# Performance work log

Measured on AMD Instinct MI355X. Metric: run time of the kernel, lower is better.

Reference implementation:

```python
import jax, jax.numpy as jnp
import numpy as np

EPS = 1e-12  # F.normalize default eps


def setup_inputs() -> dict:
    key = jax.random.key(0)
    k1, k2, k3, k4 = jax.random.split(key, 4)
    B, C, H, W = 8, 256, 128, 128
    N, T = 100, 6
    return {
        "visual_features": jax.random.normal(k1, (B, C, H, W), dtype=jnp.float32),
        "text_embeddings": jax.random.normal(k2, (T, C), dtype=jnp.float32),
        "masks": jax.random.uniform(k3, (B, N, H, W), dtype=jnp.float32),
        "class_labels": jax.random.randint(k4, (B, N), 0, 7),
        "temperature": jnp.asarray(0.07, dtype=jnp.float32),
    }


def reference(visual_features, text_embeddings, masks, class_labels, temperature):
    # visual_features: (B,C,H,W); text_embeddings: (T,C); masks: (B,N,H,W); class_labels: (B,N)
    T = text_embeddings.shape[0]
    # masks already at (H,W): bilinear resize to same size is identity -> just threshold
    mask_bin = (masks > 0.5).astype(visual_features.dtype)          # (B,N,H,W), detached
    mask_bin = jax.lax.stop_gradient(mask_bin)
    msum = mask_bin.sum(axis=(2, 3))                                 # (B,N)
    # masked sum-pool then mean (clamp denom at 1, as in torch)
    pooled = jnp.einsum('bchw,bnhw->bnc', visual_features, mask_bin)
    pooled = pooled / jnp.maximum(msum, 1.0)[..., None]              # (B,N,C)
    pooled = pooled / jnp.maximum(jnp.linalg.norm(pooled, axis=-1, keepdims=True), EPS)
    text_norm = text_embeddings / jnp.maximum(
        jnp.linalg.norm(text_embeddings, axis=-1, keepdims=True), EPS)
    sims = jnp.einsum('bnc,tc->bnt', pooled, text_norm) / jnp.abs(temperature)  # (B,N,T)
    logp = jax.nn.log_softmax(sims, axis=-1)
    tgt = jnp.clip(class_labels - 1, 0, T - 1)
    ce = -jnp.take_along_axis(logp, tgt[..., None], axis=-1)[..., 0]  # (B,N)
    valid = ((class_labels >= 1) & (class_labels <= T) & (msum >= 1.0)).astype(ce.dtype)
    cnt = valid.sum()
    loss = jnp.where(cnt > 0, (ce * valid).sum() / jnp.maximum(cnt, 1.0),
                     jnp.asarray(0.0, ce.dtype))
    return loss
```

## Files before the change

### kernel.cpp

```cpp
#include <hip/hip_runtime.h>
#include <hip/hip_bf16.h>
#include <stdint.h>

constexpr int cB  = 8;
constexpr int cC  = 256;
constexpr int cHW = 128 * 128;
constexpr int cN  = 100;
constexpr int cT  = 6;
constexpr int NPAD = 112;
constexpr int WPB = cHW / 32;
constexpr int KSLICES = 16;
constexpr int PXS = cHW / KSLICES;
constexpr int NWAVES = cB * 16 * KSLICES;

typedef __attribute__((ext_vector_type(8))) short short8;
typedef __attribute__((ext_vector_type(4))) float floatx4;

__device__ __forceinline__ unsigned pack2(float a, float b) {
    const __hip_bfloat16 ha = __float2bfloat16(a);
    const __hip_bfloat16 hb = __float2bfloat16(b);
    return (unsigned)__builtin_bit_cast(unsigned short, ha)
         | ((unsigned)__builtin_bit_cast(unsigned short, hb) << 16);
}

__global__ __launch_bounds__(256)
void mask_prep_kernel(const float* __restrict__ masks,
                      unsigned* __restrict__ bits, unsigned* __restrict__ msum)
{
    const int t = threadIdx.x, lane = t & 63, w = t >> 6;
    const int b = blockIdx.x / NPAD;
    const int n = blockIdx.x % NPAD;
    unsigned* dst = bits + ((size_t)b * NPAD + n) * WPB;

    if (n >= cN) {
        *(uint2*)(dst + t * 2) = make_uint2(0u, 0u);
        return;
    }
    const float* src = masks + ((size_t)b * cN + n) * cHW + w * 4096;
    unsigned* wdst = dst + w * 128;
    int pc = 0;
    for (int r = 0; r < 16; ++r) {
        const floatx4 v = *(const floatx4*)(src + r * 256 + lane * 4);
        const bool b0 = v.x > 0.5f, b1 = v.y > 0.5f, b2 = v.z > 0.5f, b3 = v.w > 0.5f;
        const unsigned long long B0 = __ballot(b0), B1 = __ballot(b1),
                                 B2 = __ballot(b2), B3 = __ballot(b3);
        pc += (int)b0 + (int)b1 + (int)b2 + (int)b3;
        if (lane < 8) {
            const int sh = lane * 8;
            const unsigned word =
                  (unsigned)((B0 >> sh) & 0xFFull)
                | ((unsigned)((B1 >> sh) & 0xFFull) << 8)
                | ((unsigned)((B2 >> sh) & 0xFFull) << 16)
                | ((unsigned)((B3 >> sh) & 0xFFull) << 24);
            wdst[r * 8 + lane] = word;
        }
    }
    #pragma unroll
    for (int off = 32; off > 0; off >>= 1) pc += __shfl_xor(pc, off, 64);
    __shared__ int ps[4];
    if (lane == 0) ps[w] = pc;
    __syncthreads();
    if (t == 0) msum[b * cN + n] = (unsigned)(ps[0] + ps[1] + ps[2] + ps[3]);
}

template<bool USE_PART>
__global__ __launch_bounds__(256)
void pool_kernel(const float* __restrict__ vf, const unsigned* __restrict__ bits,
                 float* __restrict__ part, float* __restrict__ pooled)
{
    const int tid  = threadIdx.x;
    const int lane = tid & 63;
    const int gw   = blockIdx.x * 4 + (tid >> 6);
    const int b    = gw >> 8;
    const int ct   = (gw >> 4) & 15;
    const int ks   = gw & 15;
    const int l15  = lane & 15;
    const int lk   = lane >> 4;
    const int lk2  = lk * 2;
    const int p0   = ks * PXS;

    const float* vrow = vf + ((size_t)(b * cC + ct * 16 + l15)) * cHW + p0 + lk * 8;
    const unsigned* brow = bits + ((size_t)b * NPAD + l15) * WPB + (p0 >> 5);

    floatx4 acc[7];
    #pragma unroll
    for (int mt = 0; mt < 7; ++mt) acc[mt] = (floatx4){0.f, 0.f, 0.f, 0.f};

    floatx4 vr[4][2];
    #pragma unroll
    for (int u = 0; u < 4; ++u) {
        vr[u][0] = *(const floatx4*)(vrow + u * 32);
        vr[u][1] = *(const floatx4*)(vrow + u * 32 + 4);
    }
    uint4 bwA[7], bwB[7];
    #pragma unroll
    for (int mt = 0; mt < 7; ++mt)
        bwA[mt] = *(const uint4*)(brow + (size_t)mt * 16 * WPB);

    auto GROUP = [&](int g, uint4 (&bw)[7], uint4 (&bwn)[7]) {
        if (g < 7) {
            #pragma unroll
            for (int mt = 0; mt < 7; ++mt)
                bwn[mt] = *(const uint4*)(brow + (size_t)mt * 16 * WPB + (g + 1) * 4);
        }
        #pragma unroll
        for (int u = 0; u < 4; ++u) {
            const int w = g * 4 + u;
            union { short8 s8; uint4 u4; } bq;
            bq.u4.x = pack2(vr[u][0].x, vr[u][0].y);
            bq.u4.y = pack2(vr[u][0].z, vr[u][0].w);
            bq.u4.z = pack2(vr[u][1].x, vr[u][1].y);
            bq.u4.w = pack2(vr[u][1].z, vr[u][1].w);
            if (g < 7) {
                vr[u][0] = *(const floatx4*)(vrow + (w + 4) * 32);
                vr[u][1] = *(const floatx4*)(vrow + (w + 4) * 32 + 4);
            }
            #pragma unroll
            for (int mt = 0; mt < 7; ++mt) {
                const unsigned word = (u == 0) ? bw[mt].x : (u == 1) ? bw[mt].y
                                    : (u == 2) ? bw[mt].z : bw[mt].w;
                const unsigned te = (word >> lk2) & 0x01010101u;
                const unsigned to = (word >> (lk2 + 1)) & 0x01010101u;
                union { short8 s8; uint4 u4; } aq;
                aq.u4.x = __umul24(__builtin_amdgcn_perm(0u, te, 0x04010400u), 0x3F80u);
                aq.u4.y = __umul24(__builtin_amdgcn_perm(0u, te, 0x04030402u), 0x3F80u);
                aq.u4.z = __umul24(__builtin_amdgcn_perm(0u, to, 0x04010400u), 0x3F80u);
                aq.u4.w = __umul24(__builtin_amdgcn_perm(0u, to, 0x04030402u), 0x3F80u);
                acc[mt] = __builtin_amdgcn_mfma_f32_16x16x32_bf16(aq.s8, bq.s8, acc[mt], 0, 0, 0);
            }
        }
    };

    for (int gp = 0; gp < 4; ++gp) {
        GROUP(2 * gp,     bwA, bwB);
        GROUP(2 * gp + 1, bwB, bwA);
    }

    if (USE_PART) {
        float* dst = part + (size_t)gw * (cN * 16);
        #pragma unroll
        for (int mt = 0; mt < 7; ++mt) {
            #pragma unroll
            for (int i = 0; i < 4; ++i) {
                const int n = mt * 16 + lk * 4 + i;
                if (n < cN) dst[n * 16 + l15] = acc[mt][i];
            }
        }
    } else {
        #pragma unroll
        for (int mt = 0; mt < 7; ++mt) {
            #pragma unroll
            for (int i = 0; i < 4; ++i) {
                const int n = mt * 16 + lk * 4 + i;
                if (n < cN)
                    atomicAdd(&pooled[((size_t)b * cN + n) * cC + ct * 16 + l15], acc[mt][i]);
            }
        }
    }
}

__device__ __forceinline__ float wred(float v) {
    #pragma unroll
    for (int off = 32; off > 0; off >>= 1) v += __shfl_xor(v, off, 64);
    return v;
}

template<bool USE_PART>
__global__ __launch_bounds__(256)
void finalize_kernel(const float* __restrict__ pp, const unsigned* __restrict__ msum,
                     const float* __restrict__ text, const int* __restrict__ labels,
                     const float* __restrict__ temp, float* __restrict__ bpart)
{
    const int lane = threadIdx.x & 63;
    const int wv   = threadIdx.x >> 6;
    const int row  = blockIdx.x * 4 + wv;
    const int b = row / cN, n = row % cN;

    floatx4 p = (floatx4){0.f, 0.f, 0.f, 0.f};
    if (USE_PART) {
        const int ct  = lane >> 2;
        const int col = (lane & 3) * 4;
        const float* src = pp + ((size_t)(b * 256 + ct * 16)) * (cN * 16) + n * 16 + col;
        #pragma unroll
        for (int kk = 0; kk < KSLICES; ++kk)
            p += *(const floatx4*)(src + (size_t)kk * (cN * 16));
    } else {
        p = *(const floatx4*)(pp + (size_t)row * cC + lane * 4);
    }

    const float m   = (float)msum[row];
    const float inv = 1.0f / fmaxf(m, 1.0f);
    p.x *= inv; p.y *= inv; p.z *= inv; p.w *= inv;

    const int c_global = USE_PART ? ((lane >> 2) * 16 + (lane & 3) * 4) : lane * 4;

    float psq = p.x * p.x + p.y * p.y + p.z * p.z + p.w * p.w;
    float dot[cT], tsq[cT];
    #pragma unroll
    for (int t = 0; t < cT; ++t) {
        const floatx4 x = *(const floatx4*)(text + (size_t)t * cC + c_global);
        dot[t] = p.x * x.x + p.y * x.y + p.z * x.z + p.w * x.w;
        tsq[t] = x.x * x.x + x.y * x.y + x.z * x.z + x.w * x.w;
    }
    psq = wred(psq);
    #pragma unroll
    for (int t = 0; t < cT; ++t) { dot[t] = wred(dot[t]); tsq[t] = wred(tsq[t]); }

    __shared__ float lce[4], lcnt[4];
    if (lane == 0) {
        const float tempv = fabsf(temp[0]);
        const float pn = fmaxf(sqrtf(psq), 1e-12f);
        float sims[cT], mx = -1e30f;
        #pragma unroll
        for (int t = 0; t < cT; ++t) {
            sims[t] = dot[t] / (pn * fmaxf(sqrtf(tsq[t]), 1e-12f)) / tempv;
            mx = fmaxf(mx, sims[t]);
        }
        float se = 0.f;
        #pragma unroll
        for (int t = 0; t < cT; ++t) se += expf(sims[t] - mx);
        const float lse = logf(se);

        const int lab = labels[row];
        const int tgt = min(max(lab - 1, 0), cT - 1);
        const float ce = -(sims[tgt] - mx - lse);
        const bool valid = (lab >= 1) && (lab <= cT) && (m >= 1.0f);
        lce[wv]  = valid ? ce : 0.f;
        lcnt[wv] = valid ? 1.f : 0.f;
    }
    __syncthreads();
    if (threadIdx.x == 0) {
        bpart[blockIdx.x * 2]     = lce[0] + lce[1] + lce[2] + lce[3];
        bpart[blockIdx.x * 2 + 1] = lcnt[0] + lcnt[1] + lcnt[2] + lcnt[3];
    }
}

__global__ __launch_bounds__(256)
void loss_kernel(const float* __restrict__ bp, float* __restrict__ out) {
    const int t = threadIdx.x, lane = t & 63, w = t >> 6;
    float ce = 0.f, cnt = 0.f;
    if (t < 200) { ce = bp[t * 2]; cnt = bp[t * 2 + 1]; }
    ce = wred(ce); cnt = wred(cnt);
    __shared__ float a[8];
    if (lane == 0) { a[w * 2] = ce; a[w * 2 + 1] = cnt; }
    __syncthreads();
    if (t == 0) {
        const float s = a[0] + a[2] + a[4] + a[6];
        const float c = a[1] + a[3] + a[5] + a[7];
        out[0] = (c > 0.f) ? s / fmaxf(c, 1.f) : 0.f;
    }
}

__global__ void zero_kernel(float* __restrict__ p, int n) {
    const int i = blockIdx.x * 256 + threadIdx.x;
    if (i < n) p[i] = 0.f;
}

extern "C" void kernel_launch(void* const* d_in, const int* in_sizes, int n_in,
                              void* d_out, int out_size, void* d_ws, size_t ws_size,
                              hipStream_t stream)
{
    const float* vf     = (const float*)d_in[0];
    const float* text   = (const float*)d_in[1];
    const float* masks  = (const float*)d_in[2];
    const int*   labels = (const int*)d_in[3];
    const float* temp   = (const float*)d_in[4];

    float*    wsf   = (float*)d_ws;
    float*    bpart = wsf;
    unsigned* msum  = (unsigned*)(wsf + 512);

    const size_t PART_FLOATS = (size_t)NWAVES * cN * 16;
    const size_t BITS_WORDS  = (size_t)cB * NPAD * WPB;

    const bool use_part =
        ws_size >= (4096 + PART_FLOATS + BITS_WORDS + 64) * sizeof(float);

    if (use_part) {
        float*    part = wsf + 4096;
        unsigned* bits = (unsigned*)(wsf + 4096 + PART_FLOATS);
        hipLaunchKernelGGL(mask_prep_kernel, dim3(cB * NPAD), dim3(256), 0, stream,
                           masks, bits, msum);
        hipLaunchKernelGGL((pool_kernel<true>), dim3(NWAVES / 4), dim3(256), 0, stream,
                           vf, bits, part, nullptr);
        hipLaunchKernelGGL((finalize_kernel<true>), dim3(cB * cN / 4), dim3(256), 0, stream,
                           part, msum, text, labels, temp, bpart);
    } else {
        float*    pooled = wsf + 4096;
        unsigned* bits   = (unsigned*)(wsf + 4096 + (size_t)cB * cN * cC);
        hipLaunchKernelGGL(zero_kernel, dim3((cB * cN * cC + 255) / 256), dim3(256), 0, stream,
                           pooled, cB * cN * cC);
        hipLaunchKernelGGL(mask_prep_kernel, dim3(cB * NPAD), dim3(256), 0, stream,
                           masks, bits, msum);
        hipLaunchKernelGGL((pool_kernel<false>), dim3(NWAVES / 4), dim3(256), 0, stream,
                           vf, bits, nullptr, pooled);
        hipLaunchKernelGGL((finalize_kernel<false>), dim3(cB * cN / 4), dim3(256), 0, stream,
                           pooled, msum, text, labels, temp, bpart);
    }
    hipLaunchKernelGGL(loss_kernel, dim3(1), dim3(256), 0, stream,
                       bpart, (float*)d_out);
}
```

Measured before the change: 57.30 us.

## Double K-slices and reduce partial sums across waves in shared memory

Each pool block now handles 4 consecutive K-slices, one per wave, with 32 slices instead of 16, so every wave covers half as many pixels. The four waves reduce their MFMA accumulators through shared memory before writing one partial per block. The finalize kernel then sums 8 partials per channel tile instead of 16. The goal is to cut partial-sum write traffic and the finalize reduction, at the cost of an LDS round trip, a barrier and less pipelining depth per wave. The mask-prep loop is also fully unrolled.

```diff
diff --git a/kernel.cpp b/kernel.cpp
--- a/kernel.cpp
+++ b/kernel.cpp
@@ -9,9 +9,11 @@
 constexpr int cT  = 6;
 constexpr int NPAD = 112;
 constexpr int WPB = cHW / 32;
-constexpr int KSLICES = 16;
+constexpr int KSLICES = 32;
 constexpr int PXS = cHW / KSLICES;
-constexpr int NWAVES = cB * 16 * KSLICES;
+constexpr int NWIN = PXS / 32;
+constexpr int NGRP = NWIN / 4;
+constexpr int NBLK = cB * 16 * (KSLICES / 4);
 
 typedef __attribute__((ext_vector_type(8))) short short8;
 typedef __attribute__((ext_vector_type(4))) float floatx4;
@@ -39,6 +41,7 @@
     const float* src = masks + ((size_t)b * cN + n) * cHW + w * 4096;
     unsigned* wdst = dst + w * 128;
     int pc = 0;
+    #pragma unroll
     for (int r = 0; r < 16; ++r) {
         const floatx4 v = *(const floatx4*)(src + r * 256 + lane * 4);
         const bool b0 = v.x > 0.5f, b1 = v.y > 0.5f, b2 = v.z > 0.5f, b3 = v.w > 0.5f;
@@ -68,12 +71,16 @@
 void pool_kernel(const float* __restrict__ vf, const unsigned* __restrict__ bits,
                  float* __restrict__ part, float* __restrict__ pooled)
 {
+    __shared__ float red[4][28][64];
+
     const int tid  = threadIdx.x;
     const int lane = tid & 63;
-    const int gw   = blockIdx.x * 4 + (tid >> 6);
-    const int b    = gw >> 8;
-    const int ct   = (gw >> 4) & 15;
-    const int ks   = gw & 15;
+    const int widx = tid >> 6;
+    const int bid  = blockIdx.x;
+    const int b    = bid >> 7;
+    const int ct   = (bid >> 3) & 15;
+    const int kg   = bid & 7;
+    const int ks   = kg * 4 + widx;
     const int l15  = lane & 15;
     const int lk   = lane >> 4;
     const int lk2  = lk * 2;
@@ -98,7 +105,7 @@
         bwA[mt] = *(const uint4*)(brow + (size_t)mt * 16 * WPB);
 
     auto GROUP = [&](int g, uint4 (&bw)[7], uint4 (&bwn)[7]) {
-        if (g < 7) {
+        if (g < NGRP - 1) {
             #pragma unroll
             for (int mt = 0; mt < 7; ++mt)
                 bwn[mt] = *(const uint4*)(brow + (size_t)mt * 16 * WPB + (g + 1) * 4);
@@ -111,7 +118,7 @@
             bq.u4.y = pack2(vr[u][0].z, vr[u][0].w);
             bq.u4.z = pack2(vr[u][1].x, vr[u][1].y);
             bq.u4.w = pack2(vr[u][1].z, vr[u][1].w);
-            if (g < 7) {
+            if (g < NGRP - 1) {
                 vr[u][0] = *(const floatx4*)(vrow + (w + 4) * 32);
                 vr[u][1] = *(const floatx4*)(vrow + (w + 4) * 32 + 4);
             }
@@ -131,30 +138,38 @@
         }
     };
 
-    for (int gp = 0; gp < 4; ++gp) {
-        GROUP(2 * gp,     bwA, bwB);
-        GROUP(2 * gp + 1, bwB, bwA);
+    GROUP(0, bwA, bwB);
+    GROUP(1, bwB, bwA);
+    GROUP(2, bwA, bwB);
+    GROUP(3, bwB, bwA);
+
+    #pragma unroll
+    for (int mt = 0; mt < 7; ++mt)
+        #pragma unroll
+        for (int i = 0; i < 4; ++i)
+            red[widx][mt * 4 + i][lane] = acc[mt][i];
+    __syncthreads();
+
+    float s[7];
+    #pragma unroll
+    for (int mt = 0; mt < 7; ++mt) {
+        const int e = mt * 4 + widx;
+        s[mt] = red[0][e][lane] + red[1][e][lane] + red[2][e][lane] + red[3][e][lane];
     }
 
     if (USE_PART) {
-        float* dst = part + (size_t)gw * (cN * 16);
+        float* dst = part + (size_t)bid * (cN * 16);
         #pragma unroll
         for (int mt = 0; mt < 7; ++mt) {
-            #pragma unroll
-            for (int i = 0; i < 4; ++i) {
-                const int n = mt * 16 + lk * 4 + i;
-                if (n < cN) dst[n * 16 + l15] = acc[mt][i];
-            }
+            const int n = mt * 16 + (lane >> 4) * 4 + widx;
+            if (n < cN) dst[n * 16 + l15] = s[mt];
         }
     } else {
         #pragma unroll
         for (int mt = 0; mt < 7; ++mt) {
-            #pragma unroll
-            for (int i = 0; i < 4; ++i) {
-                const int n = mt * 16 + lk * 4 + i;
-                if (n < cN)
-                    atomicAdd(&pooled[((size_t)b * cN + n) * cC + ct * 16 + l15], acc[mt][i]);
-            }
+            const int n = mt * 16 + (lane >> 4) * 4 + widx;
+            if (n < cN)
+                atomicAdd(&pooled[((size_t)b * cN + n) * cC + ct * 16 + l15], s[mt]);
         }
     }
 }
@@ -180,10 +195,10 @@
     if (USE_PART) {
         const int ct  = lane >> 2;
         const int col = (lane & 3) * 4;
-        const float* src = pp + ((size_t)(b * 256 + ct * 16)) * (cN * 16) + n * 16 + col;
-        #pragma unroll
-        for (int kk = 0; kk < KSLICES; ++kk)
-            p += *(const floatx4*)(src + (size_t)kk * (cN * 16));
+        const float* src = pp + ((size_t)(b * 16 + ct) * 8) * (cN * 16) + n * 16 + col;
+        #pragma unroll
+        for (int kg = 0; kg < 8; ++kg)
+            p += *(const floatx4*)(src + (size_t)kg * (cN * 16));
     } else {
         p = *(const floatx4*)(pp + (size_t)row * cC + lane * 4);
     }
@@ -270,7 +285,7 @@
     float*    bpart = wsf;
     unsigned* msum  = (unsigned*)(wsf + 512);
 
-    const size_t PART_FLOATS = (size_t)NWAVES * cN * 16;
+    const size_t PART_FLOATS = (size_t)NBLK * cN * 16;
     const size_t BITS_WORDS  = (size_t)cB * NPAD * WPB;
 
     const bool use_part =
@@ -281,7 +296,7 @@
         unsigned* bits = (unsigned*)(wsf + 4096 + PART_FLOATS);
         hipLaunchKernelGGL(mask_prep_kernel, dim3(cB * NPAD), dim3(256), 0, stream,
                            masks, bits, msum);
-        hipLaunchKernelGGL((pool_kernel<true>), dim3(NWAVES / 4), dim3(256), 0, stream,
+        hipLaunchKernelGGL((pool_kernel<true>), dim3(NBLK), dim3(256), 0, stream,
                            vf, bits, part, nullptr);
         hipLaunchKernelGGL((finalize_kernel<true>), dim3(cB * cN / 4), dim3(256), 0, stream,
                            part, msum, text, labels, temp, bpart);
@@ -292,7 +307,7 @@
                            pooled, cB * cN * cC);
         hipLaunchKernelGGL(mask_prep_kernel, dim3(cB * NPAD), dim3(256), 0, stream,
                            masks, bits, msum);
-        hipLaunchKernelGGL((pool_kernel<false>), dim3(NWAVES / 4), dim3(256), 0, stream,
+        hipLaunchKernelGGL((pool_kernel<false>), dim3(NBLK), dim3(256), 0, stream,
                            vf, bits, nullptr, pooled);
         hipLaunchKernelGGL((finalize_kernel<false>), dim3(cB * cN / 4), dim3(256), 0, stream,
                            pooled, msum, text, labels, temp, bpart);
```

After: 55.24 us. 1.04x faster.
